# Performance work log

Hardware: AMD Instinct MI355X
Metric: run time of the kernel (lower is better)

Reference implementation:

```python
import jax, jax.numpy as jnp
import numpy as np


def setup_inputs() -> dict:
    key = jax.random.key(0)
    ks = jax.random.split(key, 6)
    B, Nab, Nag, d, K = 16, 16384, 16384, 128, 10
    return {
        "H1": jax.random.normal(ks[0], (B, Nab, d), jnp.float32),
        "H2": jax.random.normal(ks[1], (B, Nag, d), jnp.float32),
        "X1": jax.random.normal(ks[2], (B, Nab, 3), jnp.float32),
        "X2": jax.random.normal(ks[3], (B, Nag, 3), jnp.float32),
        "W1": jax.random.uniform(ks[4], (K, d, d), jnp.float32),
        "W2": jax.random.uniform(ks[5], (K, d, d), jnp.float32),
    }


def _kabsch(P, Q):
    # Rigid alignment: find R (3x3), t (3,) s.t. P @ R + t ~= Q (least squares).
    c1 = P.mean(axis=0)
    c2 = Q.mean(axis=0)
    Pc = P - c1
    Qc = Q - c2
    Hm = Pc.T @ Qc  # [3,3] covariance
    U, S, Vt = jnp.linalg.svd(Hm, full_matrices=False)
    sign = jnp.sign(jnp.linalg.det(U @ Vt))
    Dm = jnp.diag(jnp.concatenate([jnp.ones(2, dtype=P.dtype), sign[None]]))
    R = U @ Dm @ Vt
    t = c2 - c1 @ R
    return P @ R + t, R, t


def reference(H1, H2, X1, X2, W1, W2):
    # Keypoint cross-attention. Faithful to torch:
    #   alpha_1k = softmax( (H1 @ W1_k @ H2.T).mean(dim=1) / sqrt(d) )
    # Using mean-over-columns identity: (H1 @ W @ H2.T).mean(1) = H1 @ W @ mean(H2,0)
    d = H1.shape[-1]
    scale = 1.0 / np.sqrt(d)
    h2bar = H2.mean(axis=1)  # [B, d]
    h1bar = H1.mean(axis=1)  # [B, d]
    v1 = jnp.einsum('kde,be->bkd', W1, h2bar)          # W1_k @ mean(H2)
    s1 = jnp.einsum('bnd,bkd->bkn', H1, v1) * scale     # [B, K, Nab]
    a1 = jax.nn.softmax(s1, axis=-1)
    Y1 = jnp.einsum('bkn,bnc->bkc', a1, X1)             # [B, K, 3]
    v2 = jnp.einsum('kde,be->bkd', W2, h1bar)
    s2 = jnp.einsum('bmd,bkd->bkm', H2, v2) * scale     # [B, K, Nag]
    a2 = jax.nn.softmax(s2, axis=-1)
    Y2 = jnp.einsum('bkm,bmc->bkc', a2, X2)             # [B, K, 3]
    Y1_aligned, R, t = jax.vmap(_kabsch)(Y1, Y2)
    return jnp.stack([Y1, Y2, Y1_aligned], axis=1)      # [B, 3, K, 3]
```

## Files before the change

kernel.cpp:

```cpp
#include <hip/hip_runtime.h>
#include <math.h>

#define NB 16
#define NN 16384
#define DD 128
#define KK 10

#define WS_FLOATS 46336

__global__ __launch_bounds__(256) void k_means(const float* __restrict__ H1,
                                               const float* __restrict__ H2,
                                               float* __restrict__ hsum) {
    int bi = blockIdx.x;
    int t = bi >> 10;
    int rem = bi & 1023;
    int b = rem >> 6;
    int chunk = rem & 63;
    const float* src = (t ? H2 : H1) + ((size_t)b * NN + (size_t)chunk * 256) * DD;
    const float4* src4 = (const float4*)src;
    int tid = threadIdx.x;
    float4 s = make_float4(0.f, 0.f, 0.f, 0.f);
#pragma unroll 8
    for (int i = 0; i < 32; ++i) {
        float4 x = src4[i * 256 + tid];
        s.x += x.x; s.y += x.y; s.z += x.z; s.w += x.w;
    }
    s.x += __shfl_xor(s.x, 32);
    s.y += __shfl_xor(s.y, 32);
    s.z += __shfl_xor(s.z, 32);
    s.w += __shfl_xor(s.w, 32);
    __shared__ float red[4][32][4];
    int wave = tid >> 6, lane = tid & 63;
    if (lane < 32) {
        red[wave][lane][0] = s.x; red[wave][lane][1] = s.y;
        red[wave][lane][2] = s.z; red[wave][lane][3] = s.w;
    }
    __syncthreads();
    if (tid < 32) {
        float t0 = 0.f, t1 = 0.f, t2 = 0.f, t3 = 0.f;
#pragma unroll
        for (int w = 0; w < 4; ++w) {
            t0 += red[w][tid][0]; t1 += red[w][tid][1];
            t2 += red[w][tid][2]; t3 += red[w][tid][3];
        }
        float* dst = hsum + (size_t)(t * NB + b) * DD + tid * 4;
        atomicAdd(dst + 0, t0);
        atomicAdd(dst + 1, t1);
        atomicAdd(dst + 2, t2);
        atomicAdd(dst + 3, t3);
    }
}

__global__ __launch_bounds__(128) void k_v(const float* __restrict__ W1,
                                           const float* __restrict__ W2,
                                           const float* __restrict__ hsum,
                                           float* __restrict__ v) {
    int bi = blockIdx.x;
    int p = bi / 160;
    int rem = bi % 160;
    int b = rem / 10;
    int k = rem % 10;
    const float* W = (p ? W2 : W1) + (size_t)k * DD * DD;
    const float* hb = hsum + (size_t)((1 - p) * NB + b) * DD;
    __shared__ float4 h_s[32];
    int tid = threadIdx.x;
    if (tid < 32) h_s[tid] = ((const float4*)hb)[tid];
    __syncthreads();
    const float4* Wrow = (const float4*)(W + (size_t)tid * DD);
    float acc = 0.f;
#pragma unroll 8
    for (int e4 = 0; e4 < 32; ++e4) {
        float4 w4 = Wrow[e4];
        float4 h4 = h_s[e4];
        acc += w4.x * h4.x + w4.y * h4.y + w4.z * h4.z + w4.w * h4.w;
    }
    const float SCALE = (float)(1.0 / (16384.0 * 11.313708498984761));
    v[((size_t)(p * NB + b) * KK + k) * DD + tid] = acc * SCALE;
}

__global__ __launch_bounds__(256) void k_scores(const float* __restrict__ H1,
                                                const float* __restrict__ H2,
                                                const float* __restrict__ X1,
                                                const float* __restrict__ X2,
                                                const float* __restrict__ v,
                                                float* __restrict__ accg) {
    int bi = blockIdx.x;
    int p = bi >> 11;
    int rem = bi & 2047;
    int b = rem >> 7;
    int tile = rem & 127;
    int row0 = tile << 7;
    const float* H = (p ? H2 : H1) + (size_t)b * NN * DD;
    const float* X = (p ? X2 : X1) + (size_t)b * NN * 3;
    const float* vp = v + (size_t)(p * NB + b) * KK * DD;

    __shared__ float4 v_s4[KK * DD / 4];
    __shared__ float red[4][40];
    float* v_s = (float*)v_s4;

    int tid = threadIdx.x;
    for (int i = tid; i < KK * DD / 4; i += 256)
        v_s4[i] = ((const float4*)vp)[i];
    __syncthreads();

    int g = tid >> 3;
    int l = tid & 7;
    int nbase = row0 + (g << 2);

    float accs[4][KK];
#pragma unroll
    for (int r = 0; r < 4; ++r)
#pragma unroll
        for (int k = 0; k < KK; ++k) accs[r][k] = 0.f;

#pragma unroll
    for (int j = 0; j < 4; ++j) {
        float4 h[4];
#pragma unroll
        for (int r = 0; r < 4; ++r)
            h[r] = *(const float4*)(H + (size_t)(nbase + r) * DD + (j << 5) + (l << 2));
#pragma unroll
        for (int k = 0; k < KK; ++k) {
            float4 vv = *(const float4*)(v_s + k * DD + (j << 5) + (l << 2));
#pragma unroll
            for (int r = 0; r < 4; ++r)
                accs[r][k] += h[r].x * vv.x + h[r].y * vv.y + h[r].z * vv.z + h[r].w * vv.w;
        }
    }
#pragma unroll
    for (int r = 0; r < 4; ++r)
#pragma unroll
        for (int k = 0; k < KK; ++k) {
            float s = accs[r][k];
            s += __shfl_xor(s, 1);
            s += __shfl_xor(s, 2);
            s += __shfl_xor(s, 4);
            accs[r][k] = s;
        }

    float pSE[KK], pY0[KK], pY1[KK], pY2[KK];
#pragma unroll
    for (int k = 0; k < KK; ++k) { pSE[k] = 0.f; pY0[k] = 0.f; pY1[k] = 0.f; pY2[k] = 0.f; }

#pragma unroll
    for (int r = 0; r < 4; ++r) {
        int n = nbase + r;
        float x0 = X[(size_t)n * 3 + 0];
        float x1 = X[(size_t)n * 3 + 1];
        float x2 = X[(size_t)n * 3 + 2];
#pragma unroll
        for (int k = 0; k < KK; ++k) {
            float e = __expf(accs[r][k]);
            pSE[k] += e;
            pY0[k] += e * x0;
            pY1[k] += e * x1;
            pY2[k] += e * x2;
        }
    }
#pragma unroll
    for (int k = 0; k < KK; ++k) {
        pSE[k] += __shfl_xor(pSE[k], 8);  pSE[k] += __shfl_xor(pSE[k], 16);  pSE[k] += __shfl_xor(pSE[k], 32);
        pY0[k] += __shfl_xor(pY0[k], 8);  pY0[k] += __shfl_xor(pY0[k], 16);  pY0[k] += __shfl_xor(pY0[k], 32);
        pY1[k] += __shfl_xor(pY1[k], 8);  pY1[k] += __shfl_xor(pY1[k], 16);  pY1[k] += __shfl_xor(pY1[k], 32);
        pY2[k] += __shfl_xor(pY2[k], 8);  pY2[k] += __shfl_xor(pY2[k], 16);  pY2[k] += __shfl_xor(pY2[k], 32);
    }
    int wave = tid >> 6, lane = tid & 63;
    if (lane == 0) {
#pragma unroll
        for (int k = 0; k < KK; ++k) {
            red[wave][k] = pSE[k];
            red[wave][10 + k] = pY0[k];
            red[wave][20 + k] = pY1[k];
            red[wave][30 + k] = pY2[k];
        }
    }
    __syncthreads();
    if (tid < 40) {
        float s = red[0][tid] + red[1][tid] + red[2][tid] + red[3][tid];
        atomicAdd(accg + (size_t)(p * NB + b) * 40 + tid, s);
    }
}

__global__ __launch_bounds__(64) void k_final(const float* __restrict__ accg,
                                              float* __restrict__ out) {
    int b = blockIdx.x;
    int tid = threadIdx.x;
    __shared__ float Ys[2][KK][3];
    if (tid < 2 * KK * 3) {
        int p = tid / 30;
        int r = tid % 30;
        int k = r / 3;
        int c = r % 3;
        const float* a = accg + (size_t)(p * NB + b) * 40;
        float val = a[10 + c * 10 + k] / a[k];
        Ys[p][k][c] = val;
        out[((size_t)(b * 3 + p) * KK + k) * 3 + c] = val;
    }
    __syncthreads();
    if (tid == 0) {
        double P[KK][3], Q[KK][3];
        double c1[3] = {0, 0, 0}, c2[3] = {0, 0, 0};
        for (int i = 0; i < KK; ++i)
            for (int c = 0; c < 3; ++c) {
                P[i][c] = (double)Ys[0][i][c];
                Q[i][c] = (double)Ys[1][i][c];
                c1[c] += P[i][c];
                c2[c] += Q[i][c];
            }
        for (int c = 0; c < 3; ++c) { c1[c] /= KK; c2[c] /= KK; }
        double A0[3][3];
        for (int a = 0; a < 3; ++a)
            for (int c = 0; c < 3; ++c) {
                double s = 0;
                for (int i = 0; i < KK; ++i) s += (P[i][a] - c1[a]) * (Q[i][c] - c2[c]);
                A0[a][c] = s;
            }
        double Bm[3][3], V[3][3];
        for (int a = 0; a < 3; ++a)
            for (int c = 0; c < 3; ++c) { Bm[a][c] = A0[a][c]; V[a][c] = (a == c) ? 1.0 : 0.0; }
        for (int sweep = 0; sweep < 16; ++sweep)
            for (int p = 0; p < 2; ++p)
                for (int q = p + 1; q < 3; ++q) {
                    double al = 0, be = 0, ga = 0;
                    for (int r = 0; r < 3; ++r) {
                        al += Bm[r][p] * Bm[r][p];
                        be += Bm[r][q] * Bm[r][q];
                        ga += Bm[r][p] * Bm[r][q];
                    }
                    if (fabs(ga) < 1e-300) continue;
                    double zeta = (be - al) / (2.0 * ga);
                    double t = copysign(1.0, zeta) / (fabs(zeta) + sqrt(1.0 + zeta * zeta));
                    double cs = 1.0 / sqrt(1.0 + t * t);
                    double sn = cs * t;
                    for (int r = 0; r < 3; ++r) {
                        double bp = Bm[r][p], bq = Bm[r][q];
                        Bm[r][p] = cs * bp - sn * bq;
                        Bm[r][q] = sn * bp + cs * bq;
                        double vp = V[r][p], vq = V[r][q];
                        V[r][p] = cs * vp - sn * vq;
                        V[r][q] = sn * vp + cs * vq;
                    }
                }
        double sig[3];
        for (int j = 0; j < 3; ++j) {
            sig[j] = sqrt(Bm[0][j] * Bm[0][j] + Bm[1][j] * Bm[1][j] + Bm[2][j] * Bm[2][j]);
            if (sig[j] < 1e-300) sig[j] = 1e-300;
        }
        int jmin = 0;
        if (sig[1] < sig[jmin]) jmin = 1;
        if (sig[2] < sig[jmin]) jmin = 2;
        double det = A0[0][0] * (A0[1][1] * A0[2][2] - A0[1][2] * A0[2][1])
                   - A0[0][1] * (A0[1][0] * A0[2][2] - A0[1][2] * A0[2][0])
                   + A0[0][2] * (A0[1][0] * A0[2][1] - A0[1][1] * A0[2][0]);
        double sgn = (det >= 0.0) ? 1.0 : -1.0;
        double R[3][3];
        for (int a = 0; a < 3; ++a)
            for (int c = 0; c < 3; ++c) {
                double s = 0;
                for (int j = 0; j < 3; ++j) {
                    double dj = (j == jmin) ? sgn : 1.0;
                    s += dj * (Bm[a][j] / sig[j]) * V[c][j];
                }
                R[a][c] = s;
            }
        for (int i = 0; i < KK; ++i)
            for (int c = 0; c < 3; ++c) {
                double s = c2[c];
                for (int a = 0; a < 3; ++a) s += (P[i][a] - c1[a]) * R[a][c];
                out[((size_t)(b * 3 + 2) * KK + i) * 3 + c] = (float)s;
            }
    }
}

extern "C" void kernel_launch(void* const* d_in, const int* in_sizes, int n_in,
                              void* d_out, int out_size, void* d_ws, size_t ws_size,
                              hipStream_t stream) {
    const float* H1 = (const float*)d_in[0];
    const float* H2 = (const float*)d_in[1];
    const float* X1 = (const float*)d_in[2];
    const float* X2 = (const float*)d_in[3];
    const float* W1 = (const float*)d_in[4];
    const float* W2 = (const float*)d_in[5];
    float* out = (float*)d_out;
    float* ws = (float*)d_ws;
    float* hsum = ws;
    float* v    = ws + 4096;
    float* accg = ws + 45056;

    hipMemsetAsync(d_ws, 0, WS_FLOATS * sizeof(float), stream);
    hipLaunchKernelGGL(k_means,  dim3(2048), dim3(256), 0, stream, H1, H2, hsum);
    hipLaunchKernelGGL(k_v,      dim3(320),  dim3(128), 0, stream, W1, W2, hsum, v);
    hipLaunchKernelGGL(k_scores, dim3(4096), dim3(256), 0, stream, H1, H2, X1, X2, v, accg);
    hipLaunchKernelGGL(k_final,  dim3(16),   dim3(64),  0, stream, accg, out);
}
```

Measured before the change: 380.1 us.

## Fuse H1 mean into H1 score pass to drop one full read of H1

The schedule becomes: compute the mean of H2 only, build v1, then run a score pass over H1 that also accumulates H1's column sums, then build v2 and run the H2 score pass. This removes one full read of H1 (128 MB), which is the dominant HBM traffic. The score kernel is also restructured so each 16-lane group holds v in registers and processes one row per step with a software-prefetched next row, instead of staging v in LDS. The cost is two extra dependent launches, more shuffles per row, and only one lane in sixteen doing the exp work.

New measurement: 400.6 us. +5.4%, slower.

```diff
diff --git a/kernel.cpp b/kernel.cpp
--- a/kernel.cpp
+++ b/kernel.cpp
@@ -8,58 +8,65 @@
 
 #define WS_FLOATS 46336
 
-__global__ __launch_bounds__(256) void k_means(const float* __restrict__ H1,
-                                               const float* __restrict__ H2,
+
+__global__ __launch_bounds__(256) void k_mean2(const float* __restrict__ H2,
                                                float* __restrict__ hsum) {
-    int bi = blockIdx.x;
-    int t = bi >> 10;
-    int rem = bi & 1023;
-    int b = rem >> 6;
-    int chunk = rem & 63;
-    const float* src = (t ? H2 : H1) + ((size_t)b * NN + (size_t)chunk * 256) * DD;
-    const float4* src4 = (const float4*)src;
-    int tid = threadIdx.x;
-    float4 s = make_float4(0.f, 0.f, 0.f, 0.f);
-#pragma unroll 8
-    for (int i = 0; i < 32; ++i) {
-        float4 x = src4[i * 256 + tid];
-        s.x += x.x; s.y += x.y; s.z += x.z; s.w += x.w;
-    }
-    s.x += __shfl_xor(s.x, 32);
-    s.y += __shfl_xor(s.y, 32);
-    s.z += __shfl_xor(s.z, 32);
-    s.w += __shfl_xor(s.w, 32);
-    __shared__ float red[4][32][4];
+    int tid = threadIdx.x, b = blockIdx.x;
+    int batch = b >> 7, sub = b & 127;
+    int c0 = tid & 15;
+    int rofs = sub * 16 + (tid >> 4);
+    const float4* H4 = (const float4*)H2 + (size_t)batch * (NN * (DD / 4));
+
+    float4 a0 = make_float4(0.f, 0.f, 0.f, 0.f), a1 = a0;
+    float4 h0 = H4[(size_t)rofs * 32 + c0];
+    float4 h1 = H4[(size_t)rofs * 32 + c0 + 16];
+#pragma unroll
+    for (int s = 0; s < 8; ++s) {
+        float4 g0, g1;
+        if (s < 7) {
+            int rn = (s + 1) * 2048 + rofs;
+            g0 = H4[(size_t)rn * 32 + c0];
+            g1 = H4[(size_t)rn * 32 + c0 + 16];
+        } else {
+            g0 = make_float4(0.f, 0.f, 0.f, 0.f); g1 = g0;
+        }
+        a0.x += h0.x; a0.y += h0.y; a0.z += h0.z; a0.w += h0.w;
+        a1.x += h1.x; a1.y += h1.y; a1.z += h1.z; a1.w += h1.w;
+        h0 = g0; h1 = g1;
+    }
+    a0.x += __shfl_xor(a0.x, 16); a0.x += __shfl_xor(a0.x, 32);
+    a0.y += __shfl_xor(a0.y, 16); a0.y += __shfl_xor(a0.y, 32);
+    a0.z += __shfl_xor(a0.z, 16); a0.z += __shfl_xor(a0.z, 32);
+    a0.w += __shfl_xor(a0.w, 16); a0.w += __shfl_xor(a0.w, 32);
+    a1.x += __shfl_xor(a1.x, 16); a1.x += __shfl_xor(a1.x, 32);
+    a1.y += __shfl_xor(a1.y, 16); a1.y += __shfl_xor(a1.y, 32);
+    a1.z += __shfl_xor(a1.z, 16); a1.z += __shfl_xor(a1.z, 32);
+    a1.w += __shfl_xor(a1.w, 16); a1.w += __shfl_xor(a1.w, 32);
+
+    __shared__ float4 cred[4][32];
     int wave = tid >> 6, lane = tid & 63;
-    if (lane < 32) {
-        red[wave][lane][0] = s.x; red[wave][lane][1] = s.y;
-        red[wave][lane][2] = s.z; red[wave][lane][3] = s.w;
+    if (lane < 16) {
+        cred[wave][lane] = a0;
+        cred[wave][lane + 16] = a1;
     }
     __syncthreads();
     if (tid < 32) {
-        float t0 = 0.f, t1 = 0.f, t2 = 0.f, t3 = 0.f;
-#pragma unroll
-        for (int w = 0; w < 4; ++w) {
-            t0 += red[w][tid][0]; t1 += red[w][tid][1];
-            t2 += red[w][tid][2]; t3 += red[w][tid][3];
-        }
-        float* dst = hsum + (size_t)(t * NB + b) * DD + tid * 4;
-        atomicAdd(dst + 0, t0);
-        atomicAdd(dst + 1, t1);
-        atomicAdd(dst + 2, t2);
-        atomicAdd(dst + 3, t3);
+        float4 s0 = cred[0][tid], s1 = cred[1][tid], s2 = cred[2][tid], s3 = cred[3][tid];
+        float* dst = hsum + (size_t)(NB + batch) * DD + tid * 4;
+        atomicAdd(dst + 0, s0.x + s1.x + s2.x + s3.x);
+        atomicAdd(dst + 1, s0.y + s1.y + s2.y + s3.y);
+        atomicAdd(dst + 2, s0.z + s1.z + s2.z + s3.z);
+        atomicAdd(dst + 3, s0.w + s1.w + s2.w + s3.w);
     }
 }
 
 __global__ __launch_bounds__(128) void k_v(const float* __restrict__ W1,
                                            const float* __restrict__ W2,
                                            const float* __restrict__ hsum,
-                                           float* __restrict__ v) {
+                                           float* __restrict__ v, int p) {
     int bi = blockIdx.x;
-    int p = bi / 160;
-    int rem = bi % 160;
-    int b = rem / 10;
-    int k = rem % 10;
+    int b = bi / 10;
+    int k = bi % 10;
     const float* W = (p ? W2 : W1) + (size_t)k * DD * DD;
     const float* hb = hsum + (size_t)((1 - p) * NB + b) * DD;
     __shared__ float4 h_s[32];
@@ -78,92 +85,87 @@
     v[((size_t)(p * NB + b) * KK + k) * DD + tid] = acc * SCALE;
 }
 
-__global__ __launch_bounds__(256) void k_scores(const float* __restrict__ H1,
-                                                const float* __restrict__ H2,
-                                                const float* __restrict__ X1,
-                                                const float* __restrict__ X2,
-                                                const float* __restrict__ v,
-                                                float* __restrict__ accg) {
-    int bi = blockIdx.x;
-    int p = bi >> 11;
-    int rem = bi & 2047;
-    int b = rem >> 7;
-    int tile = rem & 127;
-    int row0 = tile << 7;
-    const float* H = (p ? H2 : H1) + (size_t)b * NN * DD;
-    const float* X = (p ? X2 : X1) + (size_t)b * NN * 3;
-    const float* vp = v + (size_t)(p * NB + b) * KK * DD;
-
-    __shared__ float4 v_s4[KK * DD / 4];
+__global__ __launch_bounds__(256) void k_pass(const float* __restrict__ H,
+                                              const float* __restrict__ X,
+                                              const float* __restrict__ v,
+                                              float* __restrict__ accg,
+                                              float* __restrict__ hsumout,
+                                              int do_sum) {
+    int tid = threadIdx.x, b = blockIdx.x;
+    int batch = b >> 7, sub = b & 127;
+    int c0 = tid & 15;
+    int rofs = sub * 16 + (tid >> 4);
+    const float4* H4 = (const float4*)H + (size_t)batch * (NN * (DD / 4));
+    const float* Xb = X + (size_t)batch * NN * 3;
+    const float4* v4 = (const float4*)(v + (size_t)batch * KK * DD);
+
+    float4 va[KK], vb[KK];
+#pragma unroll
+    for (int k = 0; k < KK; ++k) {
+        va[k] = v4[k * 32 + c0];
+        vb[k] = v4[k * 32 + c0 + 16];
+    }
+
+    float pSE[KK], pY0[KK], pY1[KK], pY2[KK];
+#pragma unroll
+    for (int k = 0; k < KK; ++k) { pSE[k] = 0.f; pY0[k] = 0.f; pY1[k] = 0.f; pY2[k] = 0.f; }
+    float4 cs0 = make_float4(0.f, 0.f, 0.f, 0.f), cs1 = cs0;
+
+    float4 h0 = H4[(size_t)rofs * 32 + c0];
+    float4 h1 = H4[(size_t)rofs * 32 + c0 + 16];
+    float x0 = Xb[rofs * 3 + 0], x1 = Xb[rofs * 3 + 1], x2 = Xb[rofs * 3 + 2];
+
+#pragma unroll
+    for (int s = 0; s < 8; ++s) {
+        float4 g0, g1;
+        float y0, y1, y2;
+        if (s < 7) {
+            int rn = (s + 1) * 2048 + rofs;
+            g0 = H4[(size_t)rn * 32 + c0];
+            g1 = H4[(size_t)rn * 32 + c0 + 16];
+            y0 = Xb[rn * 3 + 0]; y1 = Xb[rn * 3 + 1]; y2 = Xb[rn * 3 + 2];
+        } else {
+            g0 = make_float4(0.f, 0.f, 0.f, 0.f); g1 = g0;
+            y0 = 0.f; y1 = 0.f; y2 = 0.f;
+        }
+        float sc[KK];
+#pragma unroll
+        for (int k = 0; k < KK; ++k)
+            sc[k] = h0.x * va[k].x + h0.y * va[k].y + h0.z * va[k].z + h0.w * va[k].w
+                  + h1.x * vb[k].x + h1.y * vb[k].y + h1.z * vb[k].z + h1.w * vb[k].w;
+#pragma unroll
+        for (int k = 0; k < KK; ++k) {
+            sc[k] += __shfl_xor(sc[k], 1);
+            sc[k] += __shfl_xor(sc[k], 2);
+            sc[k] += __shfl_xor(sc[k], 4);
+            sc[k] += __shfl_xor(sc[k], 8);
+        }
+        if (c0 == 0) {
+#pragma unroll
+            for (int k = 0; k < KK; ++k) {
+                float e = __expf(sc[k]);
+                pSE[k] += e;
+                pY0[k] += e * x0;
+                pY1[k] += e * x1;
+                pY2[k] += e * x2;
+            }
+        }
+        if (do_sum) {
+            cs0.x += h0.x; cs0.y += h0.y; cs0.z += h0.z; cs0.w += h0.w;
+            cs1.x += h1.x; cs1.y += h1.y; cs1.z += h1.z; cs1.w += h1.w;
+        }
+        h0 = g0; h1 = g1; x0 = y0; x1 = y1; x2 = y2;
+    }
+
+#pragma unroll
+    for (int k = 0; k < KK; ++k) {
+        pSE[k] += __shfl_xor(pSE[k], 16); pSE[k] += __shfl_xor(pSE[k], 32);
+        pY0[k] += __shfl_xor(pY0[k], 16); pY0[k] += __shfl_xor(pY0[k], 32);
+        pY1[k] += __shfl_xor(pY1[k], 16); pY1[k] += __shfl_xor(pY1[k], 32);
+        pY2[k] += __shfl_xor(pY2[k], 16); pY2[k] += __shfl_xor(pY2[k], 32);
+    }
     __shared__ float red[4][40];
-    float* v_s = (float*)v_s4;
-
-    int tid = threadIdx.x;
-    for (int i = tid; i < KK * DD / 4; i += 256)
-        v_s4[i] = ((const float4*)vp)[i];
-    __syncthreads();
-
-    int g = tid >> 3;
-    int l = tid & 7;
-    int nbase = row0 + (g << 2);
-
-    float accs[4][KK];
-#pragma unroll
-    for (int r = 0; r < 4; ++r)
-#pragma unroll
-        for (int k = 0; k < KK; ++k) accs[r][k] = 0.f;
-
-#pragma unroll
-    for (int j = 0; j < 4; ++j) {
-        float4 h[4];
-#pragma unroll
-        for (int r = 0; r < 4; ++r)
-            h[r] = *(const float4*)(H + (size_t)(nbase + r) * DD + (j << 5) + (l << 2));
-#pragma unroll
-        for (int k = 0; k < KK; ++k) {
-            float4 vv = *(const float4*)(v_s + k * DD + (j << 5) + (l << 2));
-#pragma unroll
-            for (int r = 0; r < 4; ++r)
-                accs[r][k] += h[r].x * vv.x + h[r].y * vv.y + h[r].z * vv.z + h[r].w * vv.w;
-        }
-    }
-#pragma unroll
-    for (int r = 0; r < 4; ++r)
-#pragma unroll
-        for (int k = 0; k < KK; ++k) {
-            float s = accs[r][k];
-            s += __shfl_xor(s, 1);
-            s += __shfl_xor(s, 2);
-            s += __shfl_xor(s, 4);
-            accs[r][k] = s;
-        }
-
-    float pSE[KK], pY0[KK], pY1[KK], pY2[KK];
-#pragma unroll
-    for (int k = 0; k < KK; ++k) { pSE[k] = 0.f; pY0[k] = 0.f; pY1[k] = 0.f; pY2[k] = 0.f; }
-
-#pragma unroll
-    for (int r = 0; r < 4; ++r) {
-        int n = nbase + r;
-        float x0 = X[(size_t)n * 3 + 0];
-        float x1 = X[(size_t)n * 3 + 1];
-        float x2 = X[(size_t)n * 3 + 2];
-#pragma unroll
-        for (int k = 0; k < KK; ++k) {
-            float e = __expf(accs[r][k]);
-            pSE[k] += e;
-            pY0[k] += e * x0;
-            pY1[k] += e * x1;
-            pY2[k] += e * x2;
-        }
-    }
-#pragma unroll
-    for (int k = 0; k < KK; ++k) {
-        pSE[k] += __shfl_xor(pSE[k], 8);  pSE[k] += __shfl_xor(pSE[k], 16);  pSE[k] += __shfl_xor(pSE[k], 32);
-        pY0[k] += __shfl_xor(pY0[k], 8);  pY0[k] += __shfl_xor(pY0[k], 16);  pY0[k] += __shfl_xor(pY0[k], 32);
-        pY1[k] += __shfl_xor(pY1[k], 8);  pY1[k] += __shfl_xor(pY1[k], 16);  pY1[k] += __shfl_xor(pY1[k], 32);
-        pY2[k] += __shfl_xor(pY2[k], 8);  pY2[k] += __shfl_xor(pY2[k], 16);  pY2[k] += __shfl_xor(pY2[k], 32);
-    }
+    __shared__ float4 cred[4][32];
     int wave = tid >> 6, lane = tid & 63;
     if (lane == 0) {
 #pragma unroll
@@ -174,10 +176,33 @@
             red[wave][30 + k] = pY2[k];
         }
     }
+    if (do_sum) {
+        cs0.x += __shfl_xor(cs0.x, 16); cs0.x += __shfl_xor(cs0.x, 32);
+        cs0.y += __shfl_xor(cs0.y, 16); cs0.y += __shfl_xor(cs0.y, 32);
+        cs0.z += __shfl_xor(cs0.z, 16); cs0.z += __shfl_xor(cs0.z, 32);
+        cs0.w += __shfl_xor(cs0.w, 16); cs0.w += __shfl_xor(cs0.w, 32);
+        cs1.x += __shfl_xor(cs1.x, 16); cs1.x += __shfl_xor(cs1.x, 32);
+        cs1.y += __shfl_xor(cs1.y, 16); cs1.y += __shfl_xor(cs1.y, 32);
+        cs1.z += __shfl_xor(cs1.z, 16); cs1.z += __shfl_xor(cs1.z, 32);
+        cs1.w += __shfl_xor(cs1.w, 16); cs1.w += __shfl_xor(cs1.w, 32);
+        if (lane < 16) {
+            cred[wave][lane] = cs0;
+            cred[wave][lane + 16] = cs1;
+        }
+    }
     __syncthreads();
     if (tid < 40) {
-        float s = red[0][tid] + red[1][tid] + red[2][tid] + red[3][tid];
-        atomicAdd(accg + (size_t)(p * NB + b) * 40 + tid, s);
+        float ssum = red[0][tid] + red[1][tid] + red[2][tid] + red[3][tid];
+        atomicAdd(accg + (size_t)batch * 40 + tid, ssum);
+    }
+    if (do_sum && tid >= 64 && tid < 96) {
+        int c = tid - 64;
+        float4 s0 = cred[0][c], s1 = cred[1][c], s2 = cred[2][c], s3 = cred[3][c];
+        float* dst = hsumout + (size_t)batch * DD + c * 4;
+        atomicAdd(dst + 0, s0.x + s1.x + s2.x + s3.x);
+        atomicAdd(dst + 1, s0.y + s1.y + s2.y + s3.y);
+        atomicAdd(dst + 2, s0.z + s1.z + s2.z + s3.z);
+        atomicAdd(dst + 3, s0.w + s1.w + s2.w + s3.w);
     }
 }
 
@@ -288,8 +313,12 @@
     float* accg = ws + 45056;
 
     hipMemsetAsync(d_ws, 0, WS_FLOATS * sizeof(float), stream);
-    hipLaunchKernelGGL(k_means,  dim3(2048), dim3(256), 0, stream, H1, H2, hsum);
-    hipLaunchKernelGGL(k_v,      dim3(320),  dim3(128), 0, stream, W1, W2, hsum, v);
-    hipLaunchKernelGGL(k_scores, dim3(4096), dim3(256), 0, stream, H1, H2, X1, X2, v, accg);
-    hipLaunchKernelGGL(k_final,  dim3(16),   dim3(64),  0, stream, accg, out);
-}
+    hipLaunchKernelGGL(k_mean2, dim3(2048), dim3(256), 0, stream, H2, hsum);
+    hipLaunchKernelGGL(k_v, dim3(160), dim3(128), 0, stream, W1, W2, hsum, v, 0);
+    hipLaunchKernelGGL(k_pass, dim3(2048), dim3(256), 0, stream,
+                       H1, X1, v, accg, hsum, 1);
+    hipLaunchKernelGGL(k_v, dim3(160), dim3(128), 0, stream, W1, W2, hsum, v, 1);
+    hipLaunchKernelGGL(k_pass, dim3(2048), dim3(256), 0, stream,
+                       H2, X2, v + (size_t)NB * KK * DD, accg + (size_t)NB * 40, hsum, 0);
+    hipLaunchKernelGGL(k_final, dim3(16), dim3(64), 0, stream, accg, out);
+}
```
